# Optimization experiments

Hardware: AMD Instinct MI355X
Metric: run time of the kernel (lower is better)

## Reference

```python
import jax, jax.numpy as jnp
import numpy as np

GRID_SIZE = 5
SPLINE_ORDER = 3
GRID_RANGE = (-1.0, 1.0)
BN_EPS = 1e-5


def _make_grid():
    h = (GRID_RANGE[1] - GRID_RANGE[0]) / GRID_SIZE
    # grid_size + 2*spline_order + 1 = 12 knots, shared across the 9 patch features
    return jnp.arange(-SPLINE_ORDER, GRID_SIZE + SPLINE_ORDER + 1, dtype=jnp.float32) * h + GRID_RANGE[0]


def _b_splines(x, grid):
    # x: (N, F) -> (N, F, grid_size + spline_order) via Cox-de Boor recursion
    x = x[..., None]
    bases = ((x >= grid[:-1]) & (x < grid[1:])).astype(x.dtype)
    for k in range(1, SPLINE_ORDER + 1):
        left = (x - grid[: -(k + 1)]) / (grid[k:-1] - grid[: -(k + 1)]) * bases[..., :-1]
        right = (grid[k + 1:] - x) / (grid[k + 1:] - grid[1:-k]) * bases[..., 1:]
        bases = left + right
    return bases


def setup_inputs() -> dict:
    key = jax.random.key(0)
    ks = jax.random.split(key, 4)
    B, C, H, W = 4, 64, 96, 96
    return {
        "x": jax.random.normal(ks[0], (B, C, H, W), dtype=jnp.float32),
        "base_weight": jax.random.normal(ks[1], (1, 9), dtype=jnp.float32) * 0.3,
        "spline_weight": jax.random.normal(ks[2], (1, 9, GRID_SIZE + SPLINE_ORDER), dtype=jnp.float32) * 0.3,
        "spline_scaler": jax.random.normal(ks[3], (1, 9), dtype=jnp.float32) * 0.3 + 1.0,
        "bn_gamma": jnp.ones((C,), dtype=jnp.float32),
        "bn_beta": jnp.zeros((C,), dtype=jnp.float32),
    }


def reference(x, base_weight, spline_weight, spline_scaler, bn_gamma, bn_beta):
    B, C, H, W = x.shape
    grid = _make_grid()
    # Per-channel depthwise 3x3 patch extraction (pad 1, stride 1), shared KANLinear(9 -> 1)
    patches = jax.lax.conv_general_dilated_patches(
        x.reshape(B * C, 1, H, W), (3, 3), (1, 1), [(1, 1), (1, 1)]
    )  # (B*C, 9, H, W)
    tok = patches.transpose(0, 2, 3, 1).reshape(-1, 9)  # (N, 9)

    base_out = jax.nn.silu(tok) @ base_weight.T  # (N, 1)
    bases = _b_splines(tok, grid)  # (N, 9, 8)
    scaled_sw = (spline_weight * spline_scaler[..., None]).reshape(1, -1)  # (1, 72)
    spline_out = bases.reshape(tok.shape[0], -1) @ scaled_sw.T  # (N, 1)

    y = (base_out + spline_out).reshape(B, C, H, W)

    # BatchNorm2d (training-mode batch statistics) + ReLU
    mean = y.mean(axis=(0, 2, 3))
    var = y.var(axis=(0, 2, 3))
    y_hat = (y - mean[None, :, None, None]) * jax.lax.rsqrt(var + BN_EPS)[None, :, None, None]
    out = jax.nn.relu(y_hat * bn_gamma[None, :, None, None] + bn_beta[None, :, None, None])
    return out
```

## Files before the change

kernel.cpp:

```cpp
#include <hip/hip_runtime.h>
#include <math.h>

#define HH 96
#define WW 96
#define CC 64
#define BB 4
#define PLANE (HH * WW)
#define NPLANES (BB * CC)
#define NPC (BB * PLANE)
#define TILE 32
#define TPL 3
#define NTILES (TPL * TPL)
#define HALO 34
#define HALO_N (HALO * HALO)
#define BLOCK 256

typedef _Float16 h2v __attribute__((ext_vector_type(2)));

static __device__ __forceinline__ float dot2h(unsigned a, unsigned b, float c) {
#if __has_builtin(__builtin_amdgcn_fdot2)
    return __builtin_amdgcn_fdot2(__builtin_bit_cast(h2v, a),
                                  __builtin_bit_cast(h2v, b), c, false);
#else
    h2v x = __builtin_bit_cast(h2v, a);
    h2v y = __builtin_bit_cast(h2v, b);
    return c + (float)x[0] * (float)y[0] + (float)x[1] * (float)y[1];
#endif
}

static __device__ __forceinline__ unsigned pk16(float a, float b) {
    return __builtin_bit_cast(unsigned, __builtin_amdgcn_cvt_pkrtz(a, b));
}


__global__ __launch_bounds__(BLOCK) void kconv_stage1(
    const float* __restrict__ x,
    const float* __restrict__ base_w,
    const float* __restrict__ spline_w,
    const float* __restrict__ spline_s,
    float* __restrict__ y,
    float2* __restrict__ part)
{
    __shared__ uint4  s_n[HALO_N];
    __shared__ float  s_sl[HALO_N];
    __shared__ unsigned s_wp[36];
    __shared__ float  s_bw[9];

    const int tid = threadIdx.x;

    if (tid < 36) {
        const int j = tid >> 2;
        const int k = tid & 3;
        const float sc = spline_s[j];
        const float w0 = spline_w[j * 8 + 2 * k]     * sc;
        const float w1 = spline_w[j * 8 + 2 * k + 1] * sc;
        s_wp[tid] = pk16(w0, w1);
    }
    if (tid < 9) s_bw[tid] = base_w[tid];

    const int plane = blockIdx.z;
    const int h0 = blockIdx.y * TILE;
    const int w0 = blockIdx.x * TILE;
    const float* xp = x + (size_t)plane * PLANE;

    for (int i = tid; i < HALO_N; i += BLOCK) {
        const int hy = i / HALO;
        const int hx = i - hy * HALO;
        const int gh = h0 + hy - 1;
        const int gw = w0 + hx - 1;
        float v = 0.0f;
        if (gh >= 0 && gh < HH && gw >= 0 && gw < WW) v = xp[gh * WW + gw];

        const float e  = __expf(-v);
        const float sl = v * __builtin_amdgcn_rcpf(1.0f + e);

        const float sp = fmaf(v, 2.5f, 2.5f);
        const float tf = floorf(sp);
        const float u  = sp - tf;
        const int   t  = (int)tf;
        const int   m  = t >> 1;
        const bool  odd = (t & 1) != 0;

        const float w1m = 1.0f - u;
        const float u2 = u * u;
        const float u3 = u2 * u;
        const float B0 = w1m * w1m * (w1m * (1.0f / 6.0f));
        const float B3 = u2 * (u * (1.0f / 6.0f));
        const float B1 = fmaf(-u2, 1.0f, fmaf(u3, 0.5f, 2.0f / 3.0f));
        const float B2 = 1.0f - B0 - B1 - B3;

        const unsigned h01 = pk16(B0, B1);
        const unsigned h23 = pk16(B2, B3);

        unsigned n[4];
        unsigned a_prev;
        {
            const int k0 = -1 - m;
            a_prev = (k0 == 0) ? h01 : ((k0 == 1) ? h23 : 0u);
        }
#pragma unroll
        for (int d = 0; d < 4; ++d) {
            const int k0 = d - m;
            const unsigned a_cur = (k0 == 0) ? h01 : ((k0 == 1) ? h23 : 0u);
            const unsigned sh = __builtin_amdgcn_alignbit(a_cur, a_prev, 16);
            n[d] = odd ? sh : a_cur;
            a_prev = a_cur;
        }

        s_n[i]  = make_uint4(n[0], n[1], n[2], n[3]);
        s_sl[i] = sl;
    }
    __syncthreads();

    unsigned wp[36];
    float bw[9];
#pragma unroll
    for (int q = 0; q < 36; ++q)
        wp[q] = __builtin_amdgcn_readfirstlane(s_wp[q]);
#pragma unroll
    for (int q = 0; q < 9; ++q)
        bw[q] = __int_as_float(__builtin_amdgcn_readfirstlane(__float_as_int(s_bw[q])));

    const int tx  = tid & 31;
    const int ty4 = (tid >> 5) * 4;

    float acc[4] = {0.0f, 0.0f, 0.0f, 0.0f};

#pragma unroll
    for (int r = 0; r < 6; ++r) {
        const int base = (ty4 + r) * HALO + tx;
        uint4 cn[3];
        float cs[3];
#pragma unroll
        for (int dw = 0; dw < 3; ++dw) {
            cn[dw] = s_n[base + dw];
            cs[dw] = s_sl[base + dw];
        }
#pragma unroll
        for (int k = 0; k < 4; ++k) {
            const int dh = r - k;
            if (dh >= 0 && dh < 3) {
#pragma unroll
                for (int dw = 0; dw < 3; ++dw) {
                    const int j = dh * 3 + dw;
                    float a = acc[k];
                    a = dot2h(cn[dw].x, wp[j * 4 + 0], a);
                    a = dot2h(cn[dw].y, wp[j * 4 + 1], a);
                    a = dot2h(cn[dw].z, wp[j * 4 + 2], a);
                    a = dot2h(cn[dw].w, wp[j * 4 + 3], a);
                    a = fmaf(bw[j], cs[dw], a);
                    acc[k] = a;
                }
            }
        }
    }

    float lsum = 0.0f, lsq = 0.0f;
    float* yp = y + (size_t)plane * PLANE + (size_t)h0 * WW + w0;
#pragma unroll
    for (int k = 0; k < 4; ++k) {
        yp[(ty4 + k) * WW + tx] = acc[k];
        lsum += acc[k];
        lsq = fmaf(acc[k], acc[k], lsq);
    }

#pragma unroll
    for (int off = 32; off; off >>= 1) {
        lsum += __shfl_down(lsum, off, 64);
        lsq  += __shfl_down(lsq,  off, 64);
    }
    __shared__ float2 red[4];
    if ((tid & 63) == 0) red[tid >> 6] = make_float2(lsum, lsq);
    __syncthreads();
    if (tid == 0) {
        const float s = red[0].x + red[1].x + red[2].x + red[3].x;
        const float q = red[0].y + red[1].y + red[2].y + red[3].y;
        part[plane * NTILES + blockIdx.y * TPL + blockIdx.x] = make_float2(s, q);
    }
}

__global__ __launch_bounds__(BLOCK) void kconv_stage2(
    float* __restrict__ y,
    const float2* __restrict__ part,
    const float* __restrict__ gamma,
    const float* __restrict__ beta)
{
    __shared__ float2 sb;
    const int tid = threadIdx.x;
    const int plane = blockIdx.x;
    const int c = plane & (CC - 1);

    if (tid < 64) {
        float s = 0.0f, q = 0.0f;
        if (tid < 36) {
            const int b = tid / 9;
            const int t = tid - b * 9;
            const float2 pp = part[(c + CC * b) * NTILES + t];
            s = pp.x; q = pp.y;
        }
#pragma unroll
        for (int off = 32; off; off >>= 1) {
            s += __shfl_down(s, off, 64);
            q += __shfl_down(q, off, 64);
        }
        if (tid == 0) {
            const float inv = 1.0f / (float)NPC;
            const float mean = s * inv;
            const float var  = q * inv - mean * mean;
            const float sc   = rsqrtf(var + 1e-5f) * gamma[c];
            sb = make_float2(sc, beta[c] - mean * sc);
        }
    }
    __syncthreads();
    const float2 sbv = sb;

    float4* yp = (float4*)(y + (size_t)plane * PLANE + (size_t)blockIdx.y * 1024);
    float4 v = yp[tid];
    v.x = fmaxf(fmaf(v.x, sbv.x, sbv.y), 0.0f);
    v.y = fmaxf(fmaf(v.y, sbv.x, sbv.y), 0.0f);
    v.z = fmaxf(fmaf(v.z, sbv.x, sbv.y), 0.0f);
    v.w = fmaxf(fmaf(v.w, sbv.x, sbv.y), 0.0f);
    yp[tid] = v;
}

extern "C" void kernel_launch(void* const* d_in, const int* in_sizes, int n_in,
                              void* d_out, int out_size, void* d_ws, size_t ws_size,
                              hipStream_t stream)
{
    const float* x        = (const float*)d_in[0];
    const float* base_w   = (const float*)d_in[1];
    const float* spline_w = (const float*)d_in[2];
    const float* spline_s = (const float*)d_in[3];
    const float* gamma    = (const float*)d_in[4];
    const float* beta     = (const float*)d_in[5];
    float* out   = (float*)d_out;
    float2* part = (float2*)d_ws;

    dim3 g1(TPL, TPL, NPLANES);
    kconv_stage1<<<g1, BLOCK, 0, stream>>>(x, base_w, spline_w, spline_s, out, part);

    dim3 g2(NPLANES, PLANE / (BLOCK * 4));
    kconv_stage2<<<g2, BLOCK, 0, stream>>>(out, part, gamma, beta);
}
```

Before: 86.60 us.

## Loop each block over three width tiles with register-prefetched halo loads

After: 86.23 us. Within noise of the previous version (-0.4%).

```diff
diff --git a/kernel.cpp b/kernel.cpp
--- a/kernel.cpp
+++ b/kernel.cpp
@@ -45,6 +45,7 @@
     __shared__ float  s_sl[HALO_N];
     __shared__ unsigned s_wp[36];
     __shared__ float  s_bw[9];
+    __shared__ float2 red[4];
 
     const int tid = threadIdx.x;
 
@@ -52,130 +53,147 @@
         const int j = tid >> 2;
         const int k = tid & 3;
         const float sc = spline_s[j];
-        const float w0 = spline_w[j * 8 + 2 * k]     * sc;
-        const float w1 = spline_w[j * 8 + 2 * k + 1] * sc;
-        s_wp[tid] = pk16(w0, w1);
+        s_wp[tid] = pk16(spline_w[j * 8 + 2 * k] * sc,
+                         spline_w[j * 8 + 2 * k + 1] * sc);
     }
     if (tid < 9) s_bw[tid] = base_w[tid];
 
-    const int plane = blockIdx.z;
-    const int h0 = blockIdx.y * TILE;
-    const int w0 = blockIdx.x * TILE;
+    const int plane = blockIdx.y;
+    const int h0 = blockIdx.x * TILE;
     const float* xp = x + (size_t)plane * PLANE;
 
-    for (int i = tid; i < HALO_N; i += BLOCK) {
-        const int hy = i / HALO;
-        const int hx = i - hy * HALO;
-        const int gh = h0 + hy - 1;
-        const int gw = w0 + hx - 1;
-        float v = 0.0f;
-        if (gh >= 0 && gh < HH && gw >= 0 && gw < WW) v = xp[gh * WW + gw];
-
-        const float e  = __expf(-v);
-        const float sl = v * __builtin_amdgcn_rcpf(1.0f + e);
-
-        const float sp = fmaf(v, 2.5f, 2.5f);
-        const float tf = floorf(sp);
-        const float u  = sp - tf;
-        const int   t  = (int)tf;
-        const int   m  = t >> 1;
-        const bool  odd = (t & 1) != 0;
-
-        const float w1m = 1.0f - u;
-        const float u2 = u * u;
-        const float u3 = u2 * u;
-        const float B0 = w1m * w1m * (w1m * (1.0f / 6.0f));
-        const float B3 = u2 * (u * (1.0f / 6.0f));
-        const float B1 = fmaf(-u2, 1.0f, fmaf(u3, 0.5f, 2.0f / 3.0f));
-        const float B2 = 1.0f - B0 - B1 - B3;
-
-        const unsigned h01 = pk16(B0, B1);
-        const unsigned h23 = pk16(B2, B3);
-
-        unsigned n[4];
-        unsigned a_prev;
-        {
-            const int k0 = -1 - m;
-            a_prev = (k0 == 0) ? h01 : ((k0 == 1) ? h23 : 0u);
-        }
-#pragma unroll
-        for (int d = 0; d < 4; ++d) {
-            const int k0 = d - m;
-            const unsigned a_cur = (k0 == 0) ? h01 : ((k0 == 1) ? h23 : 0u);
-            const unsigned sh = __builtin_amdgcn_alignbit(a_cur, a_prev, 16);
-            n[d] = odd ? sh : a_cur;
-            a_prev = a_cur;
-        }
-
-        s_n[i]  = make_uint4(n[0], n[1], n[2], n[3]);
-        s_sl[i] = sl;
-    }
-    __syncthreads();
-
-    unsigned wp[36];
-    float bw[9];
-#pragma unroll
-    for (int q = 0; q < 36; ++q)
-        wp[q] = __builtin_amdgcn_readfirstlane(s_wp[q]);
-#pragma unroll
-    for (int q = 0; q < 9; ++q)
-        bw[q] = __int_as_float(__builtin_amdgcn_readfirstlane(__float_as_int(s_bw[q])));
+    int hy[5], hx[5];
+#pragma unroll
+    for (int s = 0; s < 5; ++s) {
+        const int i = tid + s * BLOCK;
+        const int r = i / HALO;
+        hy[s] = r;
+        hx[s] = i - r * HALO;
+    }
 
     const int tx  = tid & 31;
     const int ty4 = (tid >> 5) * 4;
 
-    float acc[4] = {0.0f, 0.0f, 0.0f, 0.0f};
-
-#pragma unroll
-    for (int r = 0; r < 6; ++r) {
-        const int base = (ty4 + r) * HALO + tx;
-        uint4 cn[3];
-        float cs[3];
-#pragma unroll
-        for (int dw = 0; dw < 3; ++dw) {
-            cn[dw] = s_n[base + dw];
-            cs[dw] = s_sl[base + dw];
-        }
+    for (int wt = 0; wt < TPL; ++wt) {
+        const int w0 = wt * TILE;
+
+        float v[5];
+#pragma unroll
+        for (int s = 0; s < 5; ++s) {
+            const int gh = h0 + hy[s] - 1;
+            const int gw = w0 + hx[s] - 1;
+            const bool ok = (tid + s * BLOCK < HALO_N) &&
+                            gh >= 0 && gh < HH && gw >= 0 && gw < WW;
+            v[s] = ok ? xp[gh * WW + gw] : 0.0f;
+        }
+
+        if (wt == 0) __syncthreads();
+
+#pragma unroll
+        for (int s = 0; s < 5; ++s) {
+            const int i = tid + s * BLOCK;
+            if (i >= HALO_N) break;
+            const float vv = v[s];
+            const float e  = __expf(-vv);
+            const float sl = vv * __builtin_amdgcn_rcpf(1.0f + e);
+
+            const float sp = fmaf(vv, 2.5f, 2.5f);
+            const float tf = floorf(sp);
+            const float u  = sp - tf;
+            const int   t  = (int)tf;
+            const int   m  = t >> 1;
+            const bool  odd = (t & 1) != 0;
+
+            const float w1m = 1.0f - u;
+            const float u2 = u * u;
+            const float u3 = u2 * u;
+            const float B0 = w1m * w1m * (w1m * (1.0f / 6.0f));
+            const float B3 = u2 * (u * (1.0f / 6.0f));
+            const float B1 = fmaf(-u2, 1.0f, fmaf(u3, 0.5f, 2.0f / 3.0f));
+            const float B2 = 1.0f - B0 - B1 - B3;
+
+            const unsigned h01 = pk16(B0, B1);
+            const unsigned h23 = pk16(B2, B3);
+
+            unsigned n[4];
+            unsigned a_prev;
+            {
+                const int k0 = -1 - m;
+                a_prev = (k0 == 0) ? h01 : ((k0 == 1) ? h23 : 0u);
+            }
+#pragma unroll
+            for (int d = 0; d < 4; ++d) {
+                const int k0 = d - m;
+                const unsigned a_cur = (k0 == 0) ? h01 : ((k0 == 1) ? h23 : 0u);
+                const unsigned sh = __builtin_amdgcn_alignbit(a_cur, a_prev, 16);
+                n[d] = odd ? sh : a_cur;
+                a_prev = a_cur;
+            }
+            s_n[i]  = make_uint4(n[0], n[1], n[2], n[3]);
+            s_sl[i] = sl;
+        }
+        __syncthreads();
+
+        unsigned wp[36];
+        float bw[9];
+#pragma unroll
+        for (int q = 0; q < 36; ++q)
+            wp[q] = __builtin_amdgcn_readfirstlane(s_wp[q]);
+#pragma unroll
+        for (int q = 0; q < 9; ++q)
+            bw[q] = __int_as_float(__builtin_amdgcn_readfirstlane(__float_as_int(s_bw[q])));
+
+        float acc[4] = {0.0f, 0.0f, 0.0f, 0.0f};
+#pragma unroll
+        for (int r = 0; r < 6; ++r) {
+            const int base = (ty4 + r) * HALO + tx;
+            uint4 cn[3];
+            float cs[3];
+#pragma unroll
+            for (int dw = 0; dw < 3; ++dw) {
+                cn[dw] = s_n[base + dw];
+                cs[dw] = s_sl[base + dw];
+            }
+#pragma unroll
+            for (int k = 0; k < 4; ++k) {
+                const int dh = r - k;
+                if (dh >= 0 && dh < 3) {
+#pragma unroll
+                    for (int dw = 0; dw < 3; ++dw) {
+                        const int j = dh * 3 + dw;
+                        float a = acc[k];
+                        a = dot2h(cn[dw].x, wp[j * 4 + 0], a);
+                        a = dot2h(cn[dw].y, wp[j * 4 + 1], a);
+                        a = dot2h(cn[dw].z, wp[j * 4 + 2], a);
+                        a = dot2h(cn[dw].w, wp[j * 4 + 3], a);
+                        a = fmaf(bw[j], cs[dw], a);
+                        acc[k] = a;
+                    }
+                }
+            }
+        }
+
+        float lsum = 0.0f, lsq = 0.0f;
+        float* yp = y + (size_t)plane * PLANE + (size_t)h0 * WW + w0;
 #pragma unroll
         for (int k = 0; k < 4; ++k) {
-            const int dh = r - k;
-            if (dh >= 0 && dh < 3) {
-#pragma unroll
-                for (int dw = 0; dw < 3; ++dw) {
-                    const int j = dh * 3 + dw;
-                    float a = acc[k];
-                    a = dot2h(cn[dw].x, wp[j * 4 + 0], a);
-                    a = dot2h(cn[dw].y, wp[j * 4 + 1], a);
-                    a = dot2h(cn[dw].z, wp[j * 4 + 2], a);
-                    a = dot2h(cn[dw].w, wp[j * 4 + 3], a);
-                    a = fmaf(bw[j], cs[dw], a);
-                    acc[k] = a;
-                }
-            }
-        }
-    }
-
-    float lsum = 0.0f, lsq = 0.0f;
-    float* yp = y + (size_t)plane * PLANE + (size_t)h0 * WW + w0;
-#pragma unroll
-    for (int k = 0; k < 4; ++k) {
-        yp[(ty4 + k) * WW + tx] = acc[k];
-        lsum += acc[k];
-        lsq = fmaf(acc[k], acc[k], lsq);
-    }
-
-#pragma unroll
-    for (int off = 32; off; off >>= 1) {
-        lsum += __shfl_down(lsum, off, 64);
-        lsq  += __shfl_down(lsq,  off, 64);
-    }
-    __shared__ float2 red[4];
-    if ((tid & 63) == 0) red[tid >> 6] = make_float2(lsum, lsq);
-    __syncthreads();
-    if (tid == 0) {
-        const float s = red[0].x + red[1].x + red[2].x + red[3].x;
-        const float q = red[0].y + red[1].y + red[2].y + red[3].y;
-        part[plane * NTILES + blockIdx.y * TPL + blockIdx.x] = make_float2(s, q);
+            yp[(ty4 + k) * WW + tx] = acc[k];
+            lsum += acc[k];
+            lsq = fmaf(acc[k], acc[k], lsq);
+        }
+
+#pragma unroll
+        for (int off = 32; off; off >>= 1) {
+            lsum += __shfl_down(lsum, off, 64);
+            lsq  += __shfl_down(lsq,  off, 64);
+        }
+        if ((tid & 63) == 0) red[tid >> 6] = make_float2(lsum, lsq);
+        __syncthreads();
+        if (tid == 0) {
+            const float s = red[0].x + red[1].x + red[2].x + red[3].x;
+            const float q = red[0].y + red[1].y + red[2].y + red[3].y;
+            part[plane * NTILES + blockIdx.x * TPL + wt] = make_float2(s, q);
+        }
     }
 }
 
@@ -236,7 +254,7 @@
     float* out   = (float*)d_out;
     float2* part = (float2*)d_ws;
 
-    dim3 g1(TPL, TPL, NPLANES);
+    dim3 g1(TPL, NPLANES);
     kconv_stage1<<<g1, BLOCK, 0, stream>>>(x, base_w, spline_w, spline_s, out, part);
 
     dim3 g2(NPLANES, PLANE / (BLOCK * 4));
```
